# Kernel tuning notes

Measured on AMD Instinct MI355X. Metric: run time of the kernel, lower is better.

Reference implementation:

```python
import jax, jax.numpy as jnp
import numpy as np

B, S, DH, DF, DM = 32, 2048, 1024, 1024, 512


def setup_inputs() -> dict:
    key = jax.random.key(0)
    ks = jax.random.split(key, 7)
    s_h = 1.0 / np.sqrt(DH)
    s_f = 1.0 / np.sqrt(DF)
    s_m = 1.0 / np.sqrt(DM)
    return {
        "hidden_states": jax.random.normal(ks[0], (B, DH), jnp.float32),
        "feats": jax.random.normal(ks[1], (B, S, DF), jnp.float32),
        "W1h": jax.random.uniform(ks[2], (DM, DH), jnp.float32, -s_h, s_h),
        "b1h": jax.random.uniform(ks[3], (DM,), jnp.float32, -s_h, s_h),
        "W1f": jax.random.uniform(ks[4], (DM, DF), jnp.float32, -s_f, s_f),
        "b1f": jax.random.uniform(ks[5], (DM,), jnp.float32, -s_f, s_f),
        "w2": jax.random.uniform(ks[6], (DM,), jnp.float32, -s_m, s_m),
    }


def reference(hidden_states, feats, W1h, b1h, W1f, b1f, w2):
    # additive (Bahdanau) attention, single feature stream
    emb_h = hidden_states @ W1h.T + b1h                     # [B, DM]
    emb_f = jnp.einsum('bsd,md->bsm', feats, W1f) + b1f      # [B, S, DM]
    emb = jnp.tanh(emb_h[:, None, :] + emb_f)                # [B, S, DM]
    logits = jnp.einsum('bsm,m->bs', emb, w2)                # [B, S]
    probs = jax.nn.softmax(logits, axis=-1)                  # [B, S]
    context = jnp.einsum('bs,bsd->bd', probs, feats)         # [B, DF]
    # torch: cat(context, dim=1) -> [B, DF]; stack(probs, dim=1) -> [B, 1, S]
    return context, probs[:, None, :]
```

## Files before the change

kernel.cpp:

```cpp
#include <hip/hip_runtime.h>
#include <hip/hip_bf16.h>
#include <cstdint>
#include <cstddef>

#define B_   32
#define S_   2048
#define DH_  1024
#define DF_  1024
#define DM_  512
#define MTOT (B_ * S_)

typedef __attribute__((ext_vector_type(8))) short bf16x8;
typedef __attribute__((ext_vector_type(4))) float f32x4;

#define AS1 __attribute__((address_space(1)))
#define AS3 __attribute__((address_space(3)))

static __device__ __forceinline__ void load_lds16(const void* g, void* l) {
    __builtin_amdgcn_global_load_lds((const AS1 unsigned*)g, (AS3 unsigned*)l,
                                     16, 0, 0);
}

static __device__ __forceinline__ unsigned pack_rhu(float a, float b) {
    unsigned ua = (__float_as_uint(a) + 0x8000u) >> 16;
    unsigned ub = (__float_as_uint(b) + 0x8000u) & 0xFFFF0000u;
    return ua | ub;
}

static __device__ __forceinline__ float tanh_fast(float x) {
    float e = __expf(2.0f * x);
    return 1.0f - 2.0f / (e + 1.0f);
}

__global__ __launch_bounds__(256) void k_embh(
    const float* __restrict__ hidden, const float* __restrict__ W1h,
    const float* __restrict__ b1h, const float* __restrict__ b1f,
    float* __restrict__ embh)
{
    int b  = blockIdx.x;
    int mg = blockIdx.y;
    int t  = threadIdx.x;
    int m  = mg * 64 + (t >> 2);
    int kp = (t & 3) * 256;
    const float4* h4 = (const float4*)(hidden + (size_t)b * DH_ + kp);
    const float4* w4 = (const float4*)(W1h + (size_t)m * DH_ + kp);
    float s = 0.0f;
    #pragma unroll 8
    for (int i = 0; i < 64; ++i) {
        float4 a = h4[i];
        float4 w = w4[i];
        s += a.x * w.x + a.y * w.y + a.z * w.z + a.w * w.w;
    }
    s += __shfl_xor(s, 1);
    s += __shfl_xor(s, 2);
    if ((t & 3) == 0)
        embh[b * DM_ + m] = s + b1h[m] + b1f[m];
}

__global__ __launch_bounds__(256) void k_cvt(
    const float* __restrict__ src, unsigned short* __restrict__ dst)
{
    size_t i = (size_t)blockIdx.x * 256 + threadIdx.x;
    float4 a = ((const float4*)src)[2 * i];
    float4 b = ((const float4*)src)[2 * i + 1];
    uint4 r;
    r.x = pack_rhu(a.x, a.y);
    r.y = pack_rhu(a.z, a.w);
    r.z = pack_rhu(b.x, b.y);
    r.w = pack_rhu(b.z, b.w);
    ((uint4*)dst)[i] = r;
}

__global__ __launch_bounds__(256) void k_gemm_bf(
    const unsigned short* __restrict__ fb, const unsigned short* __restrict__ wb,
    const float* __restrict__ embh, const float* __restrict__ w2,
    float* __restrict__ plog)
{
    __shared__ bf16x8 As[4 * 128];
    __shared__ bf16x8 Bs[4 * 128];

    const int t    = threadIdx.x;
    const int lane = t & 63;
    const int w    = t >> 6;
    const int wm   = w >> 1;
    const int wn   = w & 1;
    const int quad = lane >> 4;
    const int l16  = lane & 15;

    const int blk   = blockIdx.x;
    const int panel = blk >> 5;
    const int sub   = blk & 31;
    const int bx    = sub >> 3;
    const int by    = panel * 8 + (sub & 7);

    const unsigned short* aG0 = fb + ((size_t)(by * 128) + lane) * DF_ + w * 8;
    const unsigned short* aG1 = aG0 + (size_t)64 * DF_;
    const unsigned short* bG0 = wb + ((size_t)(bx * 128) + lane) * DF_ + w * 8;
    const unsigned short* bG1 = bG0 + (size_t)64 * DF_;
    bf16x8* ldsA0 = &As[w * 128];
    bf16x8* ldsA1 = &As[w * 128 + 64];
    bf16x8* ldsB0 = &Bs[w * 128];
    bf16x8* ldsB1 = &Bs[w * 128 + 64];

    f32x4 acc[4][4];
    const f32x4 zero = {0.0f, 0.0f, 0.0f, 0.0f};
    #pragma unroll
    for (int i = 0; i < 4; ++i)
        #pragma unroll
        for (int j = 0; j < 4; ++j) acc[i][j] = zero;

    for (int kt = 0; kt < DF_ / 32; ++kt) {
        __syncthreads();
        load_lds16(aG0 + kt * 32, ldsA0);
        load_lds16(aG1 + kt * 32, ldsA1);
        load_lds16(bG0 + kt * 32, ldsB0);
        load_lds16(bG1 + kt * 32, ldsB1);
        __syncthreads();

        bf16x8 af[4], bfr[4];
        #pragma unroll
        for (int mi = 0; mi < 4; ++mi)
            af[mi] = As[quad * 128 + wm * 64 + mi * 16 + l16];
        #pragma unroll
        for (int nj = 0; nj < 4; ++nj)
            bfr[nj] = Bs[quad * 128 + wn * 64 + nj * 16 + l16];

        #pragma unroll
        for (int mi = 0; mi < 4; ++mi)
            #pragma unroll
            for (int nj = 0; nj < 4; ++nj)
                acc[mi][nj] = __builtin_amdgcn_mfma_f32_16x16x32_bf16(
                    af[mi], bfr[nj], acc[mi][nj], 0, 0, 0);
    }

    const int bIdx = by >> 4;
    float ew[4], wv[4];
    #pragma unroll
    for (int nj = 0; nj < 4; ++nj) {
        int c = bx * 128 + wn * 64 + nj * 16 + l16;
        ew[nj] = embh[bIdx * DM_ + c];
        wv[nj] = w2[c];
    }
    float* plw = plog + (size_t)(bx * 2 + wn) * MTOT + bIdx * S_;
    #pragma unroll
    for (int mi = 0; mi < 4; ++mi) {
        #pragma unroll
        for (int reg = 0; reg < 4; ++reg) {
            float p = 0.0f;
            #pragma unroll
            for (int nj = 0; nj < 4; ++nj)
                p += tanh_fast(acc[mi][nj][reg] + ew[nj]) * wv[nj];
            p += __shfl_xor(p, 1);
            p += __shfl_xor(p, 2);
            p += __shfl_xor(p, 4);
            p += __shfl_xor(p, 8);
            if (l16 == 0) {
                int rowl = wm * 64 + mi * 16 + quad * 4 + reg;
                int s = (by * 128 + rowl) & (S_ - 1);
                plw[s] = p;
            }
        }
    }
}

__global__ __launch_bounds__(256) void k_gemm_f32(
    const float* __restrict__ feats, const unsigned short* __restrict__ w1fb,
    const float* __restrict__ embh, const float* __restrict__ w2,
    float* __restrict__ plog)
{
    __shared__ bf16x8 As[4 * 128];
    __shared__ bf16x8 Bs[4 * 128];

    const int t    = threadIdx.x;
    const int lane = t & 63;
    const int w    = t >> 6;
    const int wm   = w >> 1;
    const int wn   = w & 1;
    const int quad = lane >> 4;
    const int l16  = lane & 15;
    const int blk   = blockIdx.x;
    const int panel = blk >> 5;
    const int sub   = blk & 31;
    const int bx    = sub >> 3;
    const int by    = panel * 8 + (sub & 7);

    const int sRow = t >> 1;
    const int sK   = (t & 1) * 16;
    const int c0   = sK >> 3;
    const float*          aG = feats + (size_t)(by * 128 + sRow) * DF_ + sK;
    const unsigned short* bG = w1fb  + (size_t)(bx * 128 + sRow) * DF_ + sK;

    f32x4 acc[4][4];
    const f32x4 zero = {0.0f, 0.0f, 0.0f, 0.0f};
    #pragma unroll
    for (int i = 0; i < 4; ++i)
        #pragma unroll
        for (int j = 0; j < 4; ++j) acc[i][j] = zero;

    for (int kt = 0; kt < DF_ / 32; ++kt) {
        float4 a0 = *(const float4*)(aG + kt * 32);
        float4 a1 = *(const float4*)(aG + kt * 32 + 4);
        float4 a2 = *(const float4*)(aG + kt * 32 + 8);
        float4 a3 = *(const float4*)(aG + kt * 32 + 12);
        uint4  b0 = *(const uint4*)(bG + kt * 32);
        uint4  b1 = *(const uint4*)(bG + kt * 32 + 8);

        __syncthreads();

        union { unsigned u[4]; bf16x8 v; } pa;
        pa.u[0] = pack_rhu(a0.x, a0.y);
        pa.u[1] = pack_rhu(a0.z, a0.w);
        pa.u[2] = pack_rhu(a1.x, a1.y);
        pa.u[3] = pack_rhu(a1.z, a1.w);
        As[c0 * 128 + sRow] = pa.v;
        pa.u[0] = pack_rhu(a2.x, a2.y);
        pa.u[1] = pack_rhu(a2.z, a2.w);
        pa.u[2] = pack_rhu(a3.x, a3.y);
        pa.u[3] = pack_rhu(a3.z, a3.w);
        As[(c0 + 1) * 128 + sRow] = pa.v;

        union { uint4 q; bf16x8 v; } pb;
        pb.q = b0;
        Bs[c0 * 128 + sRow] = pb.v;
        pb.q = b1;
        Bs[(c0 + 1) * 128 + sRow] = pb.v;

        __syncthreads();

        bf16x8 af[4], bfr[4];
        #pragma unroll
        for (int mi = 0; mi < 4; ++mi)
            af[mi] = As[quad * 128 + wm * 64 + mi * 16 + l16];
        #pragma unroll
        for (int nj = 0; nj < 4; ++nj)
            bfr[nj] = Bs[quad * 128 + wn * 64 + nj * 16 + l16];

        #pragma unroll
        for (int mi = 0; mi < 4; ++mi)
            #pragma unroll
            for (int nj = 0; nj < 4; ++nj)
                acc[mi][nj] = __builtin_amdgcn_mfma_f32_16x16x32_bf16(
                    af[mi], bfr[nj], acc[mi][nj], 0, 0, 0);
    }

    const int bIdx = by >> 4;
    float ew[4], wv[4];
    #pragma unroll
    for (int nj = 0; nj < 4; ++nj) {
        int c = bx * 128 + wn * 64 + nj * 16 + l16;
        ew[nj] = embh[bIdx * DM_ + c];
        wv[nj] = w2[c];
    }
    float* plw = plog + (size_t)(bx * 2 + wn) * MTOT + bIdx * S_;
    #pragma unroll
    for (int mi = 0; mi < 4; ++mi) {
        #pragma unroll
        for (int reg = 0; reg < 4; ++reg) {
            float p = 0.0f;
            #pragma unroll
            for (int nj = 0; nj < 4; ++nj)
                p += tanh_fast(acc[mi][nj][reg] + ew[nj]) * wv[nj];
            p += __shfl_xor(p, 1);
            p += __shfl_xor(p, 2);
            p += __shfl_xor(p, 4);
            p += __shfl_xor(p, 8);
            if (l16 == 0) {
                int rowl = wm * 64 + mi * 16 + quad * 4 + reg;
                int s = (by * 128 + rowl) & (S_ - 1);
                plw[s] = p;
            }
        }
    }
}

__global__ __launch_bounds__(256) void k_softmax(
    const float* __restrict__ plog, float* __restrict__ probs_out)
{
    int b = blockIdx.x;
    int t = threadIdx.x;
    float l[8];
    #pragma unroll
    for (int i = 0; i < 8; ++i) {
        int s = t + i * 256;
        float sum = 0.0f;
        #pragma unroll
        for (int p = 0; p < 8; ++p)
            sum += plog[(size_t)p * MTOT + b * S_ + s];
        l[i] = sum;
    }
    float mx = l[0];
    #pragma unroll
    for (int i = 1; i < 8; ++i) mx = fmaxf(mx, l[i]);
    #pragma unroll
    for (int off = 1; off < 64; off <<= 1) mx = fmaxf(mx, __shfl_xor(mx, off));
    __shared__ float redm[4];
    __shared__ float reds[4];
    int wid = t >> 6;
    if ((t & 63) == 0) redm[wid] = mx;
    __syncthreads();
    mx = fmaxf(fmaxf(redm[0], redm[1]), fmaxf(redm[2], redm[3]));

    float e[8];
    float es = 0.0f;
    #pragma unroll
    for (int i = 0; i < 8; ++i) {
        e[i] = __expf(l[i] - mx);
        es += e[i];
    }
    #pragma unroll
    for (int off = 1; off < 64; off <<= 1) es += __shfl_xor(es, off);
    if ((t & 63) == 0) reds[wid] = es;
    __syncthreads();
    es = reds[0] + reds[1] + reds[2] + reds[3];
    float inv = 1.0f / es;
    #pragma unroll
    for (int i = 0; i < 8; ++i)
        probs_out[b * S_ + t + i * 256] = e[i] * inv;
}

__global__ __launch_bounds__(256) void k_context_bf(
    const unsigned short* __restrict__ fb, const float* __restrict__ probs,
    float* __restrict__ ctxp)
{
    int dp = blockIdx.x * 256 + threadIdx.x;
    int b  = blockIdx.y;
    int z  = blockIdx.z;
    const unsigned* f  = (const unsigned*)(fb + ((size_t)b * S_ + z * 256) * DF_) + dp;
    const float*    pr = probs + b * S_ + z * 256;
    float a0 = 0.0f, a1 = 0.0f;
    #pragma unroll 4
    for (int i = 0; i < 256; ++i) {
        unsigned v = f[(size_t)i * (DF_ / 2)];
        float lo = __uint_as_float(v << 16);
        float hi = __uint_as_float(v & 0xFFFF0000u);
        float p = pr[i];
        a0 += p * lo;
        a1 += p * hi;
    }
    float2* o = (float2*)(ctxp + ((size_t)z * B_ + b) * DF_) + dp;
    *o = make_float2(a0, a1);
}

__global__ __launch_bounds__(256) void k_context_f32(
    const float* __restrict__ feats, const float* __restrict__ probs,
    float* __restrict__ ctxp)
{
    int d  = blockIdx.x * 256 + threadIdx.x;
    int b  = blockIdx.y;
    int z  = blockIdx.z;
    const float* f  = feats + ((size_t)b * S_ + z * 256) * DF_ + d;
    const float* pr = probs + b * S_ + z * 256;
    float acc = 0.0f;
    #pragma unroll 4
    for (int i = 0; i < 256; ++i)
        acc += pr[i] * f[(size_t)i * DF_];
    ctxp[((size_t)z * B_ + b) * DF_ + d] = acc;
}

__global__ __launch_bounds__(256) void k_ctx_red(
    const float* __restrict__ ctxp, float* __restrict__ ctx)
{
    int i = blockIdx.x * 256 + threadIdx.x;
    float s = 0.0f;
    #pragma unroll
    for (int z = 0; z < 8; ++z)
        s += ctxp[(size_t)z * B_ * DF_ + i];
    ctx[i] = s;
}

extern "C" void kernel_launch(void* const* d_in, const int* in_sizes, int n_in,
                              void* d_out, int out_size, void* d_ws, size_t ws_size,
                              hipStream_t stream)
{
    const float* hidden = (const float*)d_in[0];
    const float* feats  = (const float*)d_in[1];
    const float* W1h    = (const float*)d_in[2];
    const float* b1h    = (const float*)d_in[3];
    const float* W1f    = (const float*)d_in[4];
    const float* b1f    = (const float*)d_in[5];
    const float* w2     = (const float*)d_in[6];

    float* out   = (float*)d_out;
    float* ctx   = out;
    float* probs = out + B_ * DF_;

    char* ws = (char*)d_ws;
    float*          embh  = (float*)ws;
    unsigned short* w1fb  = (unsigned short*)(ws + (64 << 10));
    float*          plog  = (float*)(ws + (64 << 10) + (1 << 20));
    float*          ctxp  = (float*)(ws + (64 << 10) + (3 << 20));
    unsigned short* featb = (unsigned short*)(ws + (8 << 20));

    const bool big_ws = ws_size >= ((size_t)8 << 20) + ((size_t)B_ * S_ * DF_ * 2);

    k_embh<<<dim3(B_, DM_ / 64), 256, 0, stream>>>(hidden, W1h, b1h, b1f, embh);
    k_cvt<<<dim3((DM_ * DF_ / 8) / 256), 256, 0, stream>>>(W1f, w1fb);

    if (big_ws) {
        k_cvt<<<dim3(((size_t)MTOT * DF_ / 8) / 256), 256, 0, stream>>>(feats, featb);
        k_gemm_bf<<<dim3((MTOT / 128) * (DM_ / 128)), 256, 0, stream>>>(
            featb, w1fb, embh, w2, plog);
        k_softmax<<<dim3(B_), 256, 0, stream>>>(plog, probs);
        k_context_bf<<<dim3(DF_ / 512, B_, 8), 256, 0, stream>>>(featb, probs, ctxp);
    } else {
        k_gemm_f32<<<dim3((MTOT / 128) * (DM_ / 128)), 256, 0, stream>>>(
            feats, w1fb, embh, w2, plog);
        k_softmax<<<dim3(B_), 256, 0, stream>>>(plog, probs);
        k_context_f32<<<dim3(DF_ / 256, B_, 8), 256, 0, stream>>>(feats, probs, ctxp);
    }
    k_ctx_red<<<dim3(B_ * DF_ / 256), 256, 0, stream>>>(ctxp, ctx);
}
```

Before: 573.6 us.

## Triple-buffer GEMM LDS loads and vectorize context reduction with finer S split

The bf16 feature GEMM now keeps three LDS stages. Loads run two k-tiles ahead and are gated by vmcnt waits with one barrier per iteration instead of two, and wave priority is raised around the MFMA block. This is meant to hide global-to-LDS latency and cut barrier stalls. The context kernel now reads 16-byte bf16 vectors per thread over 64-row S chunks, producing 32 partial sums instead of 8, with the final reduction widened to match. The trade-offs are more LDS use, which may lower occupancy, and more partial-sum traffic.

```diff
diff --git a/kernel.cpp b/kernel.cpp
--- a/kernel.cpp
+++ b/kernel.cpp
@@ -30,6 +30,13 @@
 static __device__ __forceinline__ float tanh_fast(float x) {
     float e = __expf(2.0f * x);
     return 1.0f - 2.0f / (e + 1.0f);
+}
+
+static __device__ __forceinline__ float bflo(unsigned v) {
+    return __uint_as_float(v << 16);
+}
+static __device__ __forceinline__ float bfhi(unsigned v) {
+    return __uint_as_float(v & 0xFFFF0000u);
 }
 
 __global__ __launch_bounds__(256) void k_embh(
@@ -76,8 +83,8 @@
     const float* __restrict__ embh, const float* __restrict__ w2,
     float* __restrict__ plog)
 {
-    __shared__ bf16x8 As[4 * 128];
-    __shared__ bf16x8 Bs[4 * 128];
+    __shared__ bf16x8 As[3][4 * 128];
+    __shared__ bf16x8 Bs[3][4 * 128];
 
     const int t    = threadIdx.x;
     const int lane = t & 63;
@@ -97,10 +104,6 @@
     const unsigned short* aG1 = aG0 + (size_t)64 * DF_;
     const unsigned short* bG0 = wb + ((size_t)(bx * 128) + lane) * DF_ + w * 8;
     const unsigned short* bG1 = bG0 + (size_t)64 * DF_;
-    bf16x8* ldsA0 = &As[w * 128];
-    bf16x8* ldsA1 = &As[w * 128 + 64];
-    bf16x8* ldsB0 = &Bs[w * 128];
-    bf16x8* ldsB1 = &Bs[w * 128 + 64];
 
     f32x4 acc[4][4];
     const f32x4 zero = {0.0f, 0.0f, 0.0f, 0.0f};
@@ -109,28 +112,47 @@
         #pragma unroll
         for (int j = 0; j < 4; ++j) acc[i][j] = zero;
 
+    auto stage = [&](int kt, int buf) {
+        load_lds16(aG0 + kt * 32, &As[buf][w * 128]);
+        load_lds16(aG1 + kt * 32, &As[buf][w * 128 + 64]);
+        load_lds16(bG0 + kt * 32, &Bs[buf][w * 128]);
+        load_lds16(bG1 + kt * 32, &Bs[buf][w * 128 + 64]);
+    };
+
+    stage(0, 0);
+    stage(1, 1);
+
+    int cur = 0;
     for (int kt = 0; kt < DF_ / 32; ++kt) {
-        __syncthreads();
-        load_lds16(aG0 + kt * 32, ldsA0);
-        load_lds16(aG1 + kt * 32, ldsA1);
-        load_lds16(bG0 + kt * 32, ldsB0);
-        load_lds16(bG1 + kt * 32, ldsB1);
-        __syncthreads();
+        if (kt < DF_ / 32 - 1)
+            asm volatile("s_waitcnt vmcnt(4)" ::: "memory");
+        else
+            asm volatile("s_waitcnt vmcnt(0)" ::: "memory");
+        __builtin_amdgcn_s_barrier();
+
+        if (kt + 2 < DF_ / 32) {
+            int nxt = (cur == 0) ? 2 : cur - 1;
+            stage(kt + 2, nxt);
+        }
 
         bf16x8 af[4], bfr[4];
         #pragma unroll
         for (int mi = 0; mi < 4; ++mi)
-            af[mi] = As[quad * 128 + wm * 64 + mi * 16 + l16];
+            af[mi] = As[cur][quad * 128 + wm * 64 + mi * 16 + l16];
         #pragma unroll
         for (int nj = 0; nj < 4; ++nj)
-            bfr[nj] = Bs[quad * 128 + wn * 64 + nj * 16 + l16];
-
+            bfr[nj] = Bs[cur][quad * 128 + wn * 64 + nj * 16 + l16];
+
+        __builtin_amdgcn_s_setprio(1);
         #pragma unroll
         for (int mi = 0; mi < 4; ++mi)
             #pragma unroll
             for (int nj = 0; nj < 4; ++nj)
                 acc[mi][nj] = __builtin_amdgcn_mfma_f32_16x16x32_bf16(
                     af[mi], bfr[nj], acc[mi][nj], 0, 0, 0);
+        __builtin_amdgcn_s_setprio(0);
+
+        cur = (cur == 2) ? 0 : cur + 1;
     }
 
     const int bIdx = by >> 4;
@@ -322,23 +344,37 @@
     const unsigned short* __restrict__ fb, const float* __restrict__ probs,
     float* __restrict__ ctxp)
 {
-    int dp = blockIdx.x * 256 + threadIdx.x;
-    int b  = blockIdx.y;
-    int z  = blockIdx.z;
-    const unsigned* f  = (const unsigned*)(fb + ((size_t)b * S_ + z * 256) * DF_) + dp;
-    const float*    pr = probs + b * S_ + z * 256;
-    float a0 = 0.0f, a1 = 0.0f;
-    #pragma unroll 4
-    for (int i = 0; i < 256; ++i) {
-        unsigned v = f[(size_t)i * (DF_ / 2)];
-        float lo = __uint_as_float(v << 16);
-        float hi = __uint_as_float(v & 0xFFFF0000u);
+    int t    = threadIdx.x;
+    int b    = blockIdx.x;
+    int z    = blockIdx.y;
+    int half = t >> 7;
+    int dt   = t & 127;
+    int s0   = z * 128 + half * 64;
+
+    const uint4* f  = (const uint4*)(fb + (size_t)(b * S_ + s0) * DF_) + dt;
+    const float* pr = probs + b * S_ + s0;
+
+    float acc[8];
+    #pragma unroll
+    for (int j = 0; j < 8; ++j) acc[j] = 0.0f;
+
+    #pragma unroll 8
+    for (int i = 0; i < 64; ++i) {
+        uint4 v = f[(size_t)i * (DF_ / 8)];
         float p = pr[i];
-        a0 += p * lo;
-        a1 += p * hi;
-    }
-    float2* o = (float2*)(ctxp + ((size_t)z * B_ + b) * DF_) + dp;
-    *o = make_float2(a0, a1);
+        acc[0] += p * bflo(v.x);
+        acc[1] += p * bfhi(v.x);
+        acc[2] += p * bflo(v.y);
+        acc[3] += p * bfhi(v.y);
+        acc[4] += p * bflo(v.z);
+        acc[5] += p * bfhi(v.z);
+        acc[6] += p * bflo(v.w);
+        acc[7] += p * bfhi(v.w);
+    }
+
+    float4* o = (float4*)(ctxp + ((size_t)(z * 2 + half) * B_ + b) * DF_ + dt * 8);
+    o[0] = make_float4(acc[0], acc[1], acc[2], acc[3]);
+    o[1] = make_float4(acc[4], acc[5], acc[6], acc[7]);
 }
 
 __global__ __launch_bounds__(256) void k_context_f32(
@@ -348,11 +384,11 @@
     int d  = blockIdx.x * 256 + threadIdx.x;
     int b  = blockIdx.y;
     int z  = blockIdx.z;
-    const float* f  = feats + ((size_t)b * S_ + z * 256) * DF_ + d;
-    const float* pr = probs + b * S_ + z * 256;
+    const float* f  = feats + ((size_t)b * S_ + z * 64) * DF_ + d;
+    const float* pr = probs + b * S_ + z * 64;
     float acc = 0.0f;
     #pragma unroll 4
-    for (int i = 0; i < 256; ++i)
+    for (int i = 0; i < 64; ++i)
         acc += pr[i] * f[(size_t)i * DF_];
     ctxp[((size_t)z * B_ + b) * DF_ + d] = acc;
 }
@@ -363,7 +399,7 @@
     int i = blockIdx.x * 256 + threadIdx.x;
     float s = 0.0f;
     #pragma unroll
-    for (int z = 0; z < 8; ++z)
+    for (int z = 0; z < 32; ++z)
         s += ctxp[(size_t)z * B_ * DF_ + i];
     ctx[i] = s;
 }
@@ -401,12 +437,12 @@
         k_gemm_bf<<<dim3((MTOT / 128) * (DM_ / 128)), 256, 0, stream>>>(
             featb, w1fb, embh, w2, plog);
         k_softmax<<<dim3(B_), 256, 0, stream>>>(plog, probs);
-        k_context_bf<<<dim3(DF_ / 512, B_, 8), 256, 0, stream>>>(featb, probs, ctxp);
+        k_context_bf<<<dim3(B_, 16), 256, 0, stream>>>(featb, probs, ctxp);
     } else {
         k_gemm_f32<<<dim3((MTOT / 128) * (DM_ / 128)), 256, 0, stream>>>(
             feats, w1fb, embh, w2, plog);
         k_softmax<<<dim3(B_), 256, 0, stream>>>(plog, probs);
-        k_context_f32<<<dim3(DF_ / 256, B_, 8), 256, 0, stream>>>(feats, probs, ctxp);
+        k_context_f32<<<dim3(DF_ / 256, B_, 32), 256, 0, stream>>>(feats, probs, ctxp);
     }
     k_ctx_red<<<dim3(B_ * DF_ / 256), 256, 0, stream>>>(ctxp, ctx);
 }
```

Result: no change. 579.3 us (+1.0%).
